# Performance work log

Hardware: AMD Instinct MI355X
Metric: run time of the kernel (lower is better)

The kernel has to match this reference:

```python
import jax, jax.numpy as jnp
import numpy as np

N, E, B, IN, H = 50000, 800000, 256, 1024, 256


def setup_inputs() -> dict:
    key = jax.random.key(0)
    ks = iter(jax.random.split(key, 40))
    w = lambda *s: jax.random.normal(next(ks), s, jnp.float32) * 0.05
    z = lambda *s: jnp.zeros(s, jnp.float32)
    inp = {
        "x": jax.random.normal(next(ks), (N, IN), jnp.float32),
        "edge_index": jax.random.randint(next(ks), (2, E), 0, N),
        "batch": jnp.sort(jax.random.randint(next(ks), (N,), 0, B)),
        "y": jax.random.randint(next(ks), (B,), 0, 2),
        "perm": jax.random.permutation(next(ks), B),
        # masker params
        "m_fc_w": w(IN, H), "m_fc_b": z(H),
        "m_c1_w": w(H, H), "m_c1_b": z(H),
        "m_c2_w": w(H, H), "m_c2_b": z(H),
        "m_node_w": w(H, 1), "m_node_b": z(1),
        "m_edge_w": w(2 * H, 1), "m_edge_b": z(1),
        # gnn_c params
        "c_fc_w": w(IN, H), "c_fc_b": z(H),
        "c_c1_w": w(H, H), "c_c1_b": z(H),
        "c_c2_w": w(H, H), "c_c2_b": z(H),
        # gnn_b params
        "b_fc_w": w(IN, H), "b_fc_b": z(H),
        "b_c1_w": w(H, H), "b_c1_b": z(H),
        "b_c2_w": w(H, H), "b_c2_b": z(H),
        # classifier heads
        "mlp_c_w": w(2 * H, 2), "mlp_c_b": z(2),
        "mlp_b_w": w(2 * H, 2), "mlp_b_b": z(2),
    }
    return inp


def _gcn_conv(x, w, b, row, col, ew):
    """PyG GCNConv: linear -> add self-loops -> sym-norm -> scatter-add -> bias."""
    n = x.shape[0]
    xw = x @ w
    loop = jnp.arange(n)
    r = jnp.concatenate([row, loop])
    c = jnp.concatenate([col, loop])
    if ew is None:
        ewf = jnp.ones(r.shape[0], xw.dtype)
    else:
        ewf = jnp.concatenate([ew, jnp.ones(n, xw.dtype)])
    deg = jax.ops.segment_sum(ewf, c, num_segments=n)
    dis = jnp.where(deg > 0, jax.lax.rsqrt(jnp.maximum(deg, 1e-12)), 0.0)
    norm = dis[r] * ewf * dis[c]
    out = jax.ops.segment_sum(xw[r] * norm[:, None], c, num_segments=n)
    return out + b


def _gnn_net(x, row, col, batch, node_mask, edge_mask, fc_w, fc_b, c1w, c1b, c2w, c2b):
    h = x * node_mask
    h = h @ fc_w + fc_b
    h = jax.nn.relu(_gcn_conv(h, c1w, c1b, row, col, edge_mask))
    h = jax.nn.relu(_gcn_conv(h, c2w, c2b, row, col, edge_mask))
    s = jax.ops.segment_sum(h, batch, num_segments=B)
    cnt = jax.ops.segment_sum(jnp.ones(h.shape[0], h.dtype), batch, num_segments=B)
    return s / jnp.maximum(cnt, 1.0)[:, None]


def _ce(logits, y):
    return -jnp.take_along_axis(jax.nn.log_softmax(logits, -1), y[:, None], 1)[:, 0]


def _gce(logits, y, q=0.7):
    p = jax.nn.softmax(logits, -1)
    yg = jnp.take_along_axis(p, y[:, None], 1)[:, 0]
    return _ce(logits, y) * (jax.lax.stop_gradient(yg) ** q) * q


def reference(x, edge_index, batch, y, perm,
              m_fc_w, m_fc_b, m_c1_w, m_c1_b, m_c2_w, m_c2_b,
              m_node_w, m_node_b, m_edge_w, m_edge_b,
              c_fc_w, c_fc_b, c_c1_w, c_c1_b, c_c2_w, c_c2_b,
              b_fc_w, b_fc_b, b_c1_w, b_c1_b, b_c2_w, b_c2_b,
              mlp_c_w, mlp_c_b, mlp_b_w, mlp_b_b):
    sg = jax.lax.stop_gradient
    row, col = edge_index[0], edge_index[1]

    # ---- GCNMasker (dropout = eval identity) ----
    h = x @ m_fc_w + m_fc_b
    h = jax.nn.relu(_gcn_conv(h, m_c1_w, m_c1_b, row, col, None))
    h = jax.nn.relu(_gcn_conv(h, m_c2_w, m_c2_b, row, col, None))
    node_score_c = jax.nn.sigmoid(h @ m_node_w + m_node_b)          # [N,1]
    # cat([x[row],x[col]]) @ W == (x @ W_top)[row] + (x @ W_bot)[col]
    es = (h @ m_edge_w[:H])[row] + (h @ m_edge_w[H:])[col] + m_edge_b
    edge_score_c = jax.nn.sigmoid(es)                               # [E,1]
    edge_score_b = 1.0 - edge_score_c
    node_score_b = 1.0 - node_score_c

    score_c = _gnn_net(x, row, col, batch, node_score_c, edge_score_c[:, 0],
                       c_fc_w, c_fc_b, c_c1_w, c_c1_b, c_c2_w, c_c2_b)  # [B,H]
    score_b = _gnn_net(x, row, col, batch, node_score_b, edge_score_b[:, 0],
                       b_fc_w, b_fc_b, b_c1_w, b_c1_b, b_c2_w, b_c2_b)  # [B,H]

    z_c = jnp.concatenate([score_c, sg(score_b)], axis=1)
    z_b = jnp.concatenate([sg(score_c), score_b], axis=1)
    pred_c = z_c @ mlp_c_w + mlp_c_b
    pred_b = z_b @ mlp_b_w + mlp_b_b

    loss_dis = _ce(pred_c, y).mean() + _gce(pred_b, y).mean()

    z_b_swap = score_b[perm]
    label_swap = y[perm]
    z_mix_conflict = jnp.concatenate([score_c, sg(z_b_swap)], axis=1)
    z_mix_align = jnp.concatenate([sg(score_c), z_b_swap], axis=1)
    pred_mix_conflict = z_mix_conflict @ mlp_c_w + mlp_c_b
    pred_mix_align = z_mix_align @ mlp_b_w + mlp_b_b
    loss_swap = _ce(pred_mix_conflict, y).mean() + _gce(pred_mix_align, label_swap).mean()

    lambda_swap = 15.0
    loss = loss_dis + lambda_swap * loss_swap
    return pred_c, loss
```

## Files before the change

### kernel.cpp

```cpp
#include <hip/hip_runtime.h>
#include <cstdint>
#include <cstddef>

#define N_NODES 50000
#define N_EDGES 800000
#define NB      256
#define IN_DIM  1024
#define HDIM    256

typedef __attribute__((ext_vector_type(8))) short bf16x8;
typedef __attribute__((ext_vector_type(4))) short s4v;
typedef __attribute__((ext_vector_type(4))) float f32x4;

__device__ __forceinline__ float sigmoidf_(float v) { return 1.0f / (1.0f + expf(-v)); }

__device__ __forceinline__ short f2bf(float f) {
    unsigned u = __float_as_uint(f);
    unsigned r = (u + 0x7FFFu + ((u >> 16) & 1u)) >> 16;
    return (short)r;
}
__device__ __forceinline__ float bf2f(short s) {
    return __uint_as_float(((unsigned)(unsigned short)s) << 16);
}

__global__ void k_hist(const int* __restrict__ col, int* __restrict__ cnt, int n) {
    int e = blockIdx.x * 256 + threadIdx.x;
    if (e < n) atomicAdd(&cnt[col[e]], 1);
}

__global__ void k_scan1(const int* __restrict__ cnt, int* __restrict__ ptr,
                        int* __restrict__ bsums, int n) {
    __shared__ int sh[256];
    int t = threadIdx.x;
    int base = blockIdx.x * 2048 + t * 8;
    int v[8]; int s = 0;
#pragma unroll
    for (int i = 0; i < 8; ++i) { int idx = base + i; v[i] = (idx < n) ? cnt[idx] : 0; s += v[i]; }
    sh[t] = s;
    __syncthreads();
    for (int off = 1; off < 256; off <<= 1) {
        int x = (t >= off) ? sh[t - off] : 0;
        __syncthreads();
        sh[t] += x;
        __syncthreads();
    }
    int excl = sh[t] - s;
    if (t == 255) bsums[blockIdx.x] = sh[255];
    int run = excl;
#pragma unroll
    for (int i = 0; i < 8; ++i) { int idx = base + i; if (idx < n) ptr[idx] = run; run += v[i]; }
}

__global__ void k_scan2(int* __restrict__ bsums, int nb, int* __restrict__ ptr_n) {
    if (threadIdx.x == 0 && blockIdx.x == 0) {
        int run = 0;
        for (int i = 0; i < nb; ++i) { int v = bsums[i]; bsums[i] = run; run += v; }
        ptr_n[0] = run;
    }
}

__global__ void k_scan3(int* __restrict__ ptr, const int* __restrict__ bsums, int n) {
    int base = blockIdx.x * 2048 + threadIdx.x * 8;
    int add = bsums[blockIdx.x];
#pragma unroll
    for (int i = 0; i < 8; ++i) { int idx = base + i; if (idx < n) ptr[idx] += add; }
}

__global__ void k_copy_int(const int* __restrict__ a, int* __restrict__ b, int n) {
    int i = blockIdx.x * 256 + threadIdx.x;
    if (i < n) b[i] = a[i];
}

__global__ void k_scatter(const int* __restrict__ row, const int* __restrict__ col,
                          int* __restrict__ fill, int* __restrict__ src,
                          int* __restrict__ eid, int n) {
    int e = blockIdx.x * 256 + threadIdx.x;
    if (e < n) {
        int c = col[e];
        int p = atomicAdd(&fill[c], 1);
        src[p] = row[e];
        eid[p] = e;
    }
}

__global__ void k_dis1(const int* __restrict__ ptr, float* __restrict__ dis, int n) {
    int i = blockIdx.x * 256 + threadIdx.x;
    if (i < n) {
        float deg = 1.0f + (float)(ptr[i + 1] - ptr[i]);
        dis[i] = 1.0f / sqrtf(deg);
    }
}

__global__ void k_splitB(const float* __restrict__ W, short* __restrict__ bt_hi,
                         short* __restrict__ bt_lo, int K) {
    int idx = blockIdx.x * 256 + threadIdx.x;
    if (idx >= 256 * (K >> 2)) return;
    int n = idx & 255, kq = (idx >> 8) << 2;
    s4v h, l;
#pragma unroll
    for (int j = 0; j < 4; ++j) {
        float v = W[(size_t)(kq + j) * 256 + n];
        short hh = f2bf(v);
        h[j] = hh;
        l[j] = f2bf(v - bf2f(hh));
    }
    *reinterpret_cast<s4v*>(&bt_hi[(size_t)n * K + kq]) = h;
    *reinterpret_cast<s4v*>(&bt_lo[(size_t)n * K + kq]) = l;
}

template <int AMODE, int OUT, int BIAS>
__global__ __launch_bounds__(256, 2) void k_gemm(const float* __restrict__ A32,
                                                 const short* __restrict__ AHg,
                                                 const short* __restrict__ ALg,
                                                 const short* __restrict__ BtHi,
                                                 const short* __restrict__ BtLo,
                                                 const float* __restrict__ bias,
                                                 float* __restrict__ C32,
                                                 short* __restrict__ CHg,
                                                 short* __restrict__ CLg,
                                                 int M, int K) {
    constexpr int LDT = 40;
    __shared__ short Ah[128 * LDT];
    __shared__ short Al[128 * LDT];
    __shared__ short Bh[128 * LDT];
    __shared__ short Bl[128 * LDT];

    int tid = threadIdx.x;
    int lane = tid & 63;
    int wave = tid >> 6;
    int wr = wave >> 1, wc = wave & 1;
    int lr = lane & 15, kg = lane >> 4;
    int m0 = blockIdx.y * 128, n0 = blockIdx.x * 128;

    f32x4 acc[4][4] = {};

    for (int k0 = 0; k0 < K; k0 += 32) {
        if constexpr (AMODE == 0) {
#pragma unroll
            for (int i = 0; i < 4; ++i) {
                int u = tid + i * 256;
                int rowi = u >> 3, kq = (u & 7) << 2;
                int gr = m0 + rowi;
                float4 av = make_float4(0.f, 0.f, 0.f, 0.f);
                if (gr < M) av = *reinterpret_cast<const float4*>(A32 + (size_t)gr * K + (k0 + kq));
                short hx = f2bf(av.x), hy = f2bf(av.y), hz = f2bf(av.z), hw = f2bf(av.w);
                s4v h = {hx, hy, hz, hw};
                s4v l = {f2bf(av.x - bf2f(hx)), f2bf(av.y - bf2f(hy)),
                         f2bf(av.z - bf2f(hz)), f2bf(av.w - bf2f(hw))};
                *reinterpret_cast<s4v*>(&Ah[rowi * LDT + kq]) = h;
                *reinterpret_cast<s4v*>(&Al[rowi * LDT + kq]) = l;
            }
        } else {
#pragma unroll
            for (int i = 0; i < 2; ++i) {
                int u = tid + i * 256;
                int rowi = u >> 2, kc = (u & 3) << 3;
                int gr = m0 + rowi;
                int4 h = make_int4(0, 0, 0, 0), l = make_int4(0, 0, 0, 0);
                if (gr < M) {
                    size_t g = (size_t)gr * K + k0 + kc;
                    h = *reinterpret_cast<const int4*>(AHg + g);
                    l = *reinterpret_cast<const int4*>(ALg + g);
                }
                *reinterpret_cast<int4*>(&Ah[rowi * LDT + kc]) = h;
                *reinterpret_cast<int4*>(&Al[rowi * LDT + kc]) = l;
            }
        }
#pragma unroll
        for (int i = 0; i < 2; ++i) {
            int u = tid + i * 256;
            int rowi = u >> 2, cq = (u & 3) << 3;
            const size_t g = (size_t)(n0 + rowi) * K + k0 + cq;
            int4 bh = *reinterpret_cast<const int4*>(BtHi + g);
            int4 bl = *reinterpret_cast<const int4*>(BtLo + g);
            *reinterpret_cast<int4*>(&Bh[rowi * LDT + cq]) = bh;
            *reinterpret_cast<int4*>(&Bl[rowi * LDT + cq]) = bl;
        }
        __syncthreads();

        bf16x8 a_h[4], a_l[4], b_h[4], b_l[4];
#pragma unroll
        for (int i = 0; i < 4; ++i) {
            int ar = wr * 64 + i * 16 + lr;
            a_h[i] = *reinterpret_cast<const bf16x8*>(&Ah[ar * LDT + kg * 8]);
            a_l[i] = *reinterpret_cast<const bf16x8*>(&Al[ar * LDT + kg * 8]);
            int br = wc * 64 + i * 16 + lr;
            b_h[i] = *reinterpret_cast<const bf16x8*>(&Bh[br * LDT + kg * 8]);
            b_l[i] = *reinterpret_cast<const bf16x8*>(&Bl[br * LDT + kg * 8]);
        }
#pragma unroll
        for (int i = 0; i < 4; ++i)
#pragma unroll
            for (int j = 0; j < 4; ++j) {
                acc[i][j] = __builtin_amdgcn_mfma_f32_16x16x32_bf16(a_h[i], b_h[j], acc[i][j], 0, 0, 0);
                acc[i][j] = __builtin_amdgcn_mfma_f32_16x16x32_bf16(a_h[i], b_l[j], acc[i][j], 0, 0, 0);
                acc[i][j] = __builtin_amdgcn_mfma_f32_16x16x32_bf16(a_l[i], b_h[j], acc[i][j], 0, 0, 0);
            }
        __syncthreads();
    }

#pragma unroll
    for (int i = 0; i < 4; ++i) {
#pragma unroll
        for (int j = 0; j < 4; ++j) {
#pragma unroll
            for (int r = 0; r < 4; ++r) {
                int gr = m0 + wr * 64 + i * 16 + kg * 4 + r;
                if (gr >= M) continue;
                int gc = n0 + wc * 64 + j * 16 + lr;
                float v = acc[i][j][r];
                if (BIAS) v += bias[gc];
                if constexpr (OUT == 0) {
                    C32[(size_t)gr * 256 + gc] = v;
                } else {
                    short h = f2bf(v);
                    CHg[(size_t)gr * 256 + gc] = h;
                    CLg[(size_t)gr * 256 + gc] = f2bf(v - bf2f(h));
                }
            }
        }
    }
}

template <int MODE, int OUT>
__global__ __launch_bounds__(256) void k_conv(const float* __restrict__ xw,
                                              const float* __restrict__ dis,
                                              const float* __restrict__ ew,
                                              const int* __restrict__ ptr,
                                              const int* __restrict__ srcA,
                                              const int* __restrict__ eidA,
                                              const float* __restrict__ bias,
                                              float* __restrict__ out32,
                                              short* __restrict__ outH,
                                              short* __restrict__ outL) {
    int node = blockIdx.x * 4 + (threadIdx.x >> 6);
    if (node >= N_NODES) return;
    int lane = threadIdx.x & 63;
    const float4* xw4 = reinterpret_cast<const float4*>(xw);
    int s = ptr[node], e = ptr[node + 1];
    float4 acc = make_float4(0.f, 0.f, 0.f, 0.f);
    int k = s;
    for (; k + 2 <= e; k += 2) {
        int sr0 = srcA[k], sr1 = srcA[k + 1];
        float w0 = dis[sr0], w1 = dis[sr1];
        if (MODE == 1) { w0 *= ew[eidA[k]]; w1 *= ew[eidA[k + 1]]; }
        else if (MODE == 2) { w0 *= (1.0f - ew[eidA[k]]); w1 *= (1.0f - ew[eidA[k + 1]]); }
        float4 v0 = xw4[(size_t)sr0 * 64 + lane];
        float4 v1 = xw4[(size_t)sr1 * 64 + lane];
        acc.x = fmaf(w1, v1.x, fmaf(w0, v0.x, acc.x));
        acc.y = fmaf(w1, v1.y, fmaf(w0, v0.y, acc.y));
        acc.z = fmaf(w1, v1.z, fmaf(w0, v0.z, acc.z));
        acc.w = fmaf(w1, v1.w, fmaf(w0, v0.w, acc.w));
    }
    if (k < e) {
        int sr = srcA[k];
        float w = dis[sr];
        if (MODE == 1) w *= ew[eidA[k]];
        else if (MODE == 2) w *= (1.0f - ew[eidA[k]]);
        float4 v = xw4[(size_t)sr * 64 + lane];
        acc.x = fmaf(w, v.x, acc.x);
        acc.y = fmaf(w, v.y, acc.y);
        acc.z = fmaf(w, v.z, acc.z);
        acc.w = fmaf(w, v.w, acc.w);
    }
    float di = dis[node];
    float4 xv = xw4[(size_t)node * 64 + lane];
    float4 bv = reinterpret_cast<const float4*>(bias)[lane];
    float ox = fmaxf(fmaf(di, acc.x + di * xv.x, bv.x), 0.0f);
    float oy = fmaxf(fmaf(di, acc.y + di * xv.y, bv.y), 0.0f);
    float oz = fmaxf(fmaf(di, acc.z + di * xv.z, bv.z), 0.0f);
    float ow = fmaxf(fmaf(di, acc.w + di * xv.w, bv.w), 0.0f);
    size_t o4 = (size_t)node * 64 + lane;
    if constexpr (OUT == 0) {
        reinterpret_cast<float4*>(out32)[o4] = make_float4(ox, oy, oz, ow);
    } else {
        short hx = f2bf(ox), hy = f2bf(oy), hz = f2bf(oz), hw = f2bf(ow);
        s4v h = {hx, hy, hz, hw};
        s4v l = {f2bf(ox - bf2f(hx)), f2bf(oy - bf2f(hy)),
                 f2bf(oz - bf2f(hz)), f2bf(ow - bf2f(hw))};
        reinterpret_cast<s4v*>(outH)[o4] = h;
        reinterpret_cast<s4v*>(outL)[o4] = l;
    }
}

__global__ __launch_bounds__(256) void k_nodescore(const float* __restrict__ h,
                                                   const float* __restrict__ node_w,
                                                   const float* __restrict__ node_b,
                                                   const float* __restrict__ edge_w,
                                                   float* __restrict__ ns,
                                                   float* __restrict__ en1,
                                                   float* __restrict__ en2) {
    int node = blockIdx.x * 4 + (threadIdx.x >> 6);
    if (node >= N_NODES) return;
    int lane = threadIdx.x & 63;
    float4 hv = reinterpret_cast<const float4*>(h)[(size_t)node * 64 + lane];
    float4 w1 = reinterpret_cast<const float4*>(node_w)[lane];
    float4 w2 = reinterpret_cast<const float4*>(edge_w)[lane];
    float4 w3 = reinterpret_cast<const float4*>(edge_w)[64 + lane];
    float d1 = hv.x * w1.x + hv.y * w1.y + hv.z * w1.z + hv.w * w1.w;
    float d2 = hv.x * w2.x + hv.y * w2.y + hv.z * w2.z + hv.w * w2.w;
    float d3 = hv.x * w3.x + hv.y * w3.y + hv.z * w3.z + hv.w * w3.w;
#pragma unroll
    for (int off = 32; off > 0; off >>= 1) {
        d1 += __shfl_xor(d1, off);
        d2 += __shfl_xor(d2, off);
        d3 += __shfl_xor(d3, off);
    }
    if (lane == 0) {
        ns[node] = sigmoidf_(d1 + node_b[0]);
        en1[node] = d2;
        en2[node] = d3;
    }
}

__global__ void k_edgescore(const int* __restrict__ row, const int* __restrict__ col,
                            const float* __restrict__ en1, const float* __restrict__ en2,
                            const float* __restrict__ eb, float* __restrict__ esc, int n) {
    int e = blockIdx.x * 256 + threadIdx.x;
    if (e < n) esc[e] = sigmoidf_(en1[row[e]] + en2[col[e]] + eb[0]);
}

__global__ void k_degcb(const int* __restrict__ ptr, const int* __restrict__ eidA,
                        const float* __restrict__ esc, float* __restrict__ dis_c,
                        float* __restrict__ dis_b, int n) {
    int i = blockIdx.x * 256 + threadIdx.x;
    if (i >= n) return;
    int s = ptr[i], e = ptr[i + 1];
    float t = 0.f;
    for (int k = s; k < e; ++k) t += esc[eidA[k]];
    float indeg = (float)(e - s);
    dis_c[i] = 1.0f / sqrtf(1.0f + t);
    dis_b[i] = 1.0f / sqrtf(1.0f + (indeg - t));
}

template <bool INV>
__global__ void k_scale(const float* __restrict__ A, const float* __restrict__ ns,
                        const float* __restrict__ bias,
                        short* __restrict__ oh, short* __restrict__ ol) {
    int idx = blockIdx.x * 256 + threadIdx.x;
    int node = idx >> 6, q = idx & 63;
    float s = ns[node];
    if (INV) s = 1.0f - s;
    float4 v = reinterpret_cast<const float4*>(A)[idx];
    float4 b = reinterpret_cast<const float4*>(bias)[q];
    float rx = fmaf(s, v.x, b.x), ry = fmaf(s, v.y, b.y);
    float rz = fmaf(s, v.z, b.z), rw = fmaf(s, v.w, b.w);
    short hx = f2bf(rx), hy = f2bf(ry), hz = f2bf(rz), hw = f2bf(rw);
    s4v h = {hx, hy, hz, hw};
    s4v l = {f2bf(rx - bf2f(hx)), f2bf(ry - bf2f(hy)),
             f2bf(rz - bf2f(hz)), f2bf(rw - bf2f(hw))};
    reinterpret_cast<s4v*>(oh)[idx] = h;
    reinterpret_cast<s4v*>(ol)[idx] = l;
}

__global__ void k_starts(const int* __restrict__ batch, int* __restrict__ starts) {
    int b = threadIdx.x;
    if (b > NB) return;
    int lo = 0, hi = N_NODES;
    while (lo < hi) { int mid = (lo + hi) >> 1; if (batch[mid] < b) lo = mid + 1; else hi = mid; }
    starts[b] = lo;
}

__global__ __launch_bounds__(256) void k_pool(const float* __restrict__ h,
                                              const int* __restrict__ starts,
                                              float* __restrict__ out) {
    int b = blockIdx.x, ch = threadIdx.x;
    int s = starts[b], e = starts[b + 1];
    float acc = 0.f;
    for (int i = s; i < e; ++i) acc += h[(size_t)i * HDIM + ch];
    out[b * HDIM + ch] = acc / fmaxf((float)(e - s), 1.0f);
}

__global__ __launch_bounds__(64) void k_head(const float* __restrict__ score_c,
                                             const float* __restrict__ score_b,
                                             const int* __restrict__ y,
                                             const int* __restrict__ perm,
                                             const float* __restrict__ wc,
                                             const float* __restrict__ bc,
                                             const float* __restrict__ wb,
                                             const float* __restrict__ bb,
                                             float* __restrict__ pred_out,
                                             float* __restrict__ loss_part) {
    int b = blockIdx.x, lane = threadIdx.x;
    int pidx = perm[b];
    float4 vc = reinterpret_cast<const float4*>(score_c)[b * 64 + lane];
    float4 vb = reinterpret_cast<const float4*>(score_b)[b * 64 + lane];
    float4 vp = reinterpret_cast<const float4*>(score_b)[pidx * 64 + lane];
    const float4* wc4 = reinterpret_cast<const float4*>(wc);
    const float4* wb4 = reinterpret_cast<const float4*>(wb);
    float4 cA0 = wc4[lane * 2], cA1 = wc4[lane * 2 + 1];
    float4 cB0 = wc4[128 + lane * 2], cB1 = wc4[128 + lane * 2 + 1];
    float4 bA0 = wb4[lane * 2], bA1 = wb4[lane * 2 + 1];
    float4 bB0 = wb4[128 + lane * 2], bB1 = wb4[128 + lane * 2 + 1];

    float c1_0 = vc.x * cA0.x + vc.y * cA0.z + vc.z * cA1.x + vc.w * cA1.z;
    float c1_1 = vc.x * cA0.y + vc.y * cA0.w + vc.z * cA1.y + vc.w * cA1.w;
    float c2_0 = vb.x * cB0.x + vb.y * cB0.z + vb.z * cB1.x + vb.w * cB1.z;
    float c2_1 = vb.x * cB0.y + vb.y * cB0.w + vb.z * cB1.y + vb.w * cB1.w;
    float cp_0 = vp.x * cB0.x + vp.y * cB0.z + vp.z * cB1.x + vp.w * cB1.z;
    float cp_1 = vp.x * cB0.y + vp.y * cB0.w + vp.z * cB1.y + vp.w * cB1.w;
    float b1_0 = vc.x * bA0.x + vc.y * bA0.z + vc.z * bA1.x + vc.w * bA1.z;
    float b1_1 = vc.x * bA0.y + vc.y * bA0.w + vc.z * bA1.y + vc.w * bA1.w;
    float b2_0 = vb.x * bB0.x + vb.y * bB0.z + vb.z * bB1.x + vb.w * bB1.z;
    float b2_1 = vb.x * bB0.y + vb.y * bB0.w + vb.z * bB1.y + vb.w * bB1.w;
    float bp_0 = vp.x * bB0.x + vp.y * bB0.z + vp.z * bB1.x + vp.w * bB1.z;
    float bp_1 = vp.x * bB0.y + vp.y * bB0.w + vp.z * bB1.y + vp.w * bB1.w;

#pragma unroll
    for (int off = 32; off > 0; off >>= 1) {
        c1_0 += __shfl_xor(c1_0, off); c1_1 += __shfl_xor(c1_1, off);
        c2_0 += __shfl_xor(c2_0, off); c2_1 += __shfl_xor(c2_1, off);
        cp_0 += __shfl_xor(cp_0, off); cp_1 += __shfl_xor(cp_1, off);
        b1_0 += __shfl_xor(b1_0, off); b1_1 += __shfl_xor(b1_1, off);
        b2_0 += __shfl_xor(b2_0, off); b2_1 += __shfl_xor(b2_1, off);
        bp_0 += __shfl_xor(bp_0, off); bp_1 += __shfl_xor(bp_1, off);
    }
    if (lane == 0) {
        float pc0 = c1_0 + c2_0 + bc[0], pc1 = c1_1 + c2_1 + bc[1];
        float pb0 = b1_0 + b2_0 + bb[0], pb1 = b1_1 + b2_1 + bb[1];
        float pmc0 = c1_0 + cp_0 + bc[0], pmc1 = c1_1 + cp_1 + bc[1];
        float pma0 = b1_0 + bp_0 + bb[0], pma1 = b1_1 + bp_1 + bb[1];
        int yy = y[b], yp = y[pidx];

        float m1 = fmaxf(pc0, pc1);
        float lse1 = m1 + logf(expf(pc0 - m1) + expf(pc1 - m1));
        float ce_c = lse1 - (yy == 0 ? pc0 : pc1);
        float m2 = fmaxf(pb0, pb1);
        float lse2 = m2 + logf(expf(pb0 - m2) + expf(pb1 - m2));
        float ly2 = (yy == 0 ? pb0 : pb1);
        float gce_b = (lse2 - ly2) * powf(expf(ly2 - lse2), 0.7f) * 0.7f;
        float m3 = fmaxf(pmc0, pmc1);
        float lse3 = m3 + logf(expf(pmc0 - m3) + expf(pmc1 - m3));
        float ce_mc = lse3 - (yy == 0 ? pmc0 : pmc1);
        float m4 = fmaxf(pma0, pma1);
        float lse4 = m4 + logf(expf(pma0 - m4) + expf(pma1 - m4));
        float ly4 = (yp == 0 ? pma0 : pma1);
        float gce_ma = (lse4 - ly4) * powf(expf(ly4 - lse4), 0.7f) * 0.7f;

        loss_part[b] = (ce_c + gce_b + 15.0f * (ce_mc + gce_ma)) * (1.0f / (float)NB);
        pred_out[b * 2 + 0] = pc0;
        pred_out[b * 2 + 1] = pc1;
    }
}

__global__ void k_lossred(const float* __restrict__ part, float* __restrict__ out) {
    __shared__ float sh[256];
    int t = threadIdx.x;
    sh[t] = part[t];
    __syncthreads();
    for (int off = 128; off > 0; off >>= 1) {
        if (t < off) sh[t] += sh[t + off];
        __syncthreads();
    }
    if (t == 0) out[0] = sh[0];
}

extern "C" void kernel_launch(void* const* d_in, const int* in_sizes, int n_in,
                              void* d_out, int out_size, void* d_ws, size_t ws_size,
                              hipStream_t stream) {
    (void)in_sizes; (void)n_in; (void)out_size; (void)ws_size;
    const float* x      = (const float*)d_in[0];
    const int*   ei     = (const int*)d_in[1];
    const int*   batch  = (const int*)d_in[2];
    const int*   y      = (const int*)d_in[3];
    const int*   perm   = (const int*)d_in[4];
    const float* m_fc_w = (const float*)d_in[5],  *m_fc_b = (const float*)d_in[6];
    const float* m_c1_w = (const float*)d_in[7],  *m_c1_b = (const float*)d_in[8];
    const float* m_c2_w = (const float*)d_in[9],  *m_c2_b = (const float*)d_in[10];
    const float* m_nd_w = (const float*)d_in[11], *m_nd_b = (const float*)d_in[12];
    const float* m_ed_w = (const float*)d_in[13], *m_ed_b = (const float*)d_in[14];
    const float* c_fc_w = (const float*)d_in[15], *c_fc_b = (const float*)d_in[16];
    const float* c_c1_w = (const float*)d_in[17], *c_c1_b = (const float*)d_in[18];
    const float* c_c2_w = (const float*)d_in[19], *c_c2_b = (const float*)d_in[20];
    const float* b_fc_w = (const float*)d_in[21], *b_fc_b = (const float*)d_in[22];
    const float* b_c1_w = (const float*)d_in[23], *b_c1_b = (const float*)d_in[24];
    const float* b_c2_w = (const float*)d_in[25], *b_c2_b = (const float*)d_in[26];
    const float* mlp_c_w = (const float*)d_in[27], *mlp_c_b = (const float*)d_in[28];
    const float* mlp_b_w = (const float*)d_in[29], *mlp_b_b = (const float*)d_in[30];
    const int* row = ei;
    const int* col = ei + N_EDGES;

    char* p = (char*)d_ws;
    auto alloc = [&](size_t bytes) -> void* {
        uintptr_t q = ((uintptr_t)p + 255) & ~(uintptr_t)255;
        p = (char*)(q + bytes);
        return (void*)q;
    };
    float* F1 = (float*)alloc((size_t)N_NODES * HDIM * 4);
    float* F2 = (float*)alloc((size_t)N_NODES * HDIM * 4);
    short* S1h = (short*)alloc((size_t)N_NODES * HDIM * 2);
    short* S1l = (short*)alloc((size_t)N_NODES * HDIM * 2);
    short* S2h = (short*)alloc((size_t)N_NODES * HDIM * 2);
    short* S2l = (short*)alloc((size_t)N_NODES * HDIM * 2);
    int* cnt    = (int*)alloc((size_t)N_NODES * 4);
    int* ptr    = (int*)alloc((size_t)(N_NODES + 1) * 4);
    int* bsums  = (int*)alloc(32 * 4);
    int* csrc   = (int*)alloc((size_t)N_EDGES * 4);
    int* ceid   = (int*)alloc((size_t)N_EDGES * 4);
    float* dis1 = (float*)alloc((size_t)N_NODES * 4);
    float* dis_c = (float*)alloc((size_t)N_NODES * 4);
    float* dis_b = (float*)alloc((size_t)N_NODES * 4);
    float* ns   = (float*)alloc((size_t)N_NODES * 4);
    float* en1  = (float*)alloc((size_t)N_NODES * 4);
    float* en2  = (float*)alloc((size_t)N_NODES * 4);
    float* esc  = (float*)alloc((size_t)N_EDGES * 4);
    float* sc   = (float*)alloc((size_t)NB * HDIM * 4);
    float* sb   = (float*)alloc((size_t)NB * HDIM * 4);
    int* starts = (int*)alloc((size_t)(NB + 1) * 4);
    float* lpart = (float*)alloc((size_t)NB * 4);
    short* wsp[9][2];
    const int wk[9] = {IN_DIM, HDIM, HDIM, IN_DIM, HDIM, HDIM, IN_DIM, HDIM, HDIM};
    for (int i = 0; i < 9; ++i) {
        wsp[i][0] = (short*)alloc((size_t)256 * wk[i] * 2);
        wsp[i][1] = (short*)alloc((size_t)256 * wk[i] * 2);
    }
    const float* wsrc[9] = {m_fc_w, m_c1_w, m_c2_w, c_fc_w, c_c1_w, c_c2_w,
                            b_fc_w, b_c1_w, b_c2_w};

    const int EB = N_EDGES / 256;
    const int NBk = (N_NODES + 255) / 256;
    const int NW = N_NODES / 4;
    const dim3 gG(2, (N_NODES + 127) / 128);

    hipMemsetAsync(cnt, 0, (size_t)N_NODES * 4, stream);
    k_hist<<<EB, 256, 0, stream>>>(col, cnt, N_EDGES);
    k_scan1<<<25, 256, 0, stream>>>(cnt, ptr, bsums, N_NODES);
    k_scan2<<<1, 64, 0, stream>>>(bsums, 25, ptr + N_NODES);
    k_scan3<<<25, 256, 0, stream>>>(ptr, bsums, N_NODES);
    k_copy_int<<<NBk, 256, 0, stream>>>(ptr, cnt, N_NODES);
    k_scatter<<<EB, 256, 0, stream>>>(row, col, cnt, csrc, ceid, N_EDGES);
    k_dis1<<<NBk, 256, 0, stream>>>(ptr, dis1, N_NODES);
    k_starts<<<1, 512, 0, stream>>>(batch, starts);
    for (int i = 0; i < 9; ++i)
        k_splitB<<<(256 * (wk[i] >> 2) + 255) / 256, 256, 0, stream>>>(
            wsrc[i], wsp[i][0], wsp[i][1], wk[i]);

    k_gemm<0, 1, 1><<<gG, 256, 0, stream>>>(x, nullptr, nullptr, wsp[0][0], wsp[0][1],
                                            m_fc_b, nullptr, S1h, S1l, N_NODES, IN_DIM);
    k_gemm<1, 0, 0><<<gG, 256, 0, stream>>>(nullptr, S1h, S1l, wsp[1][0], wsp[1][1],
                                            nullptr, F1, nullptr, nullptr, N_NODES, HDIM);
    k_conv<0, 1><<<NW, 256, 0, stream>>>(F1, dis1, nullptr, ptr, csrc, ceid, m_c1_b,
                                         nullptr, S2h, S2l);
    k_gemm<1, 0, 0><<<gG, 256, 0, stream>>>(nullptr, S2h, S2l, wsp[2][0], wsp[2][1],
                                            nullptr, F2, nullptr, nullptr, N_NODES, HDIM);
    k_conv<0, 0><<<NW, 256, 0, stream>>>(F2, dis1, nullptr, ptr, csrc, ceid, m_c2_b,
                                         F1, nullptr, nullptr);
    k_nodescore<<<NW, 256, 0, stream>>>(F1, m_nd_w, m_nd_b, m_ed_w, ns, en1, en2);
    k_edgescore<<<EB, 256, 0, stream>>>(row, col, en1, en2, m_ed_b, esc, N_EDGES);
    k_degcb<<<NBk, 256, 0, stream>>>(ptr, ceid, esc, dis_c, dis_b, N_NODES);

    k_gemm<0, 0, 0><<<gG, 256, 0, stream>>>(x, nullptr, nullptr, wsp[3][0], wsp[3][1],
                                            nullptr, F2, nullptr, nullptr, N_NODES, IN_DIM);
    k_scale<false><<<NW, 256, 0, stream>>>(F2, ns, c_fc_b, S1h, S1l);
    k_gemm<1, 0, 0><<<gG, 256, 0, stream>>>(nullptr, S1h, S1l, wsp[4][0], wsp[4][1],
                                            nullptr, F2, nullptr, nullptr, N_NODES, HDIM);
    k_conv<1, 1><<<NW, 256, 0, stream>>>(F2, dis_c, esc, ptr, csrc, ceid, c_c1_b,
                                         nullptr, S2h, S2l);
    k_gemm<1, 0, 0><<<gG, 256, 0, stream>>>(nullptr, S2h, S2l, wsp[5][0], wsp[5][1],
                                            nullptr, F2, nullptr, nullptr, N_NODES, HDIM);
    k_conv<1, 0><<<NW, 256, 0, stream>>>(F2, dis_c, esc, ptr, csrc, ceid, c_c2_b,
                                         F1, nullptr, nullptr);
    k_pool<<<NB, 256, 0, stream>>>(F1, starts, sc);

    k_gemm<0, 0, 0><<<gG, 256, 0, stream>>>(x, nullptr, nullptr, wsp[6][0], wsp[6][1],
                                            nullptr, F2, nullptr, nullptr, N_NODES, IN_DIM);
    k_scale<true><<<NW, 256, 0, stream>>>(F2, ns, b_fc_b, S1h, S1l);
    k_gemm<1, 0, 0><<<gG, 256, 0, stream>>>(nullptr, S1h, S1l, wsp[7][0], wsp[7][1],
                                            nullptr, F2, nullptr, nullptr, N_NODES, HDIM);
    k_conv<2, 1><<<NW, 256, 0, stream>>>(F2, dis_b, esc, ptr, csrc, ceid, b_c1_b,
                                         nullptr, S2h, S2l);
    k_gemm<1, 0, 0><<<gG, 256, 0, stream>>>(nullptr, S2h, S2l, wsp[8][0], wsp[8][1],
                                            nullptr, F2, nullptr, nullptr, N_NODES, HDIM);
    k_conv<2, 0><<<NW, 256, 0, stream>>>(F2, dis_b, esc, ptr, csrc, ceid, b_c2_b,
                                         F1, nullptr, nullptr);
    k_pool<<<NB, 256, 0, stream>>>(F1, starts, sb);

    float* outp = (float*)d_out;
    k_head<<<NB, 64, 0, stream>>>(sc, sb, y, perm, mlp_c_w, mlp_c_b, mlp_b_w, mlp_b_b,
                                  outp, lpart);
    k_lossred<<<1, 256, 0, stream>>>(lpart, outp + NB * 2);
}
```

Baseline: 2.302 ms.

## Batch three input-projection GEMMs into one pass and pipeline GEMM tile loads

The three x @ fc_w projections (masker, causal, bias branches) are merged into one GEMM over a concatenated 768-column weight, so the large x matrix is read and split into bf16 hi/lo once instead of three times. The node-mask scaling and fc bias are folded into the A-load of the following hidden GEMM, which removes the separate k_scale kernel. The GEMM main loop now prefetches the next K tile into registers while the MFMAs run, and shared memory switches from padded rows to an XOR-swizzled layout. The cost is more register pressure and an extra barrier per K step, which could reduce occupancy.

Result: no change. 2.304 ms (+0.1%).

```diff
diff --git a/kernel.cpp b/kernel.cpp
--- a/kernel.cpp
+++ b/kernel.cpp
@@ -92,7 +92,7 @@
 }
 
 __global__ void k_splitB(const float* __restrict__ W, short* __restrict__ bt_hi,
-                         short* __restrict__ bt_lo, int K) {
+                         short* __restrict__ bt_lo, int K, int nOff) {
     int idx = blockIdx.x * 256 + threadIdx.x;
     if (idx >= 256 * (K >> 2)) return;
     int n = idx & 255, kq = (idx >> 8) << 2;
@@ -104,37 +104,48 @@
         h[j] = hh;
         l[j] = f2bf(v - bf2f(hh));
     }
-    *reinterpret_cast<s4v*>(&bt_hi[(size_t)n * K + kq]) = h;
-    *reinterpret_cast<s4v*>(&bt_lo[(size_t)n * K + kq]) = l;
-}
-
-template <int AMODE, int OUT, int BIAS>
+    *reinterpret_cast<s4v*>(&bt_hi[(size_t)(nOff + n) * K + kq]) = h;
+    *reinterpret_cast<s4v*>(&bt_lo[(size_t)(nOff + n) * K + kq]) = l;
+}
+
+template <int AMODE, int SCALE, int OUTK>
 __global__ __launch_bounds__(256, 2) void k_gemm(const float* __restrict__ A32,
                                                  const short* __restrict__ AHg,
                                                  const short* __restrict__ ALg,
                                                  const short* __restrict__ BtHi,
                                                  const short* __restrict__ BtLo,
-                                                 const float* __restrict__ bias,
+                                                 const float* __restrict__ nsv,
+                                                 const float* __restrict__ kbias,
+                                                 const float* __restrict__ cbias,
                                                  float* __restrict__ C32,
                                                  short* __restrict__ CHg,
                                                  short* __restrict__ CLg,
+                                                 float* __restrict__ Cf1,
+                                                 float* __restrict__ Cf2,
                                                  int M, int K) {
-    constexpr int LDT = 40;
-    __shared__ short Ah[128 * LDT];
-    __shared__ short Al[128 * LDT];
-    __shared__ short Bh[128 * LDT];
-    __shared__ short Bl[128 * LDT];
-
-    int tid = threadIdx.x;
-    int lane = tid & 63;
-    int wave = tid >> 6;
-    int wr = wave >> 1, wc = wave & 1;
-    int lr = lane & 15, kg = lane >> 4;
-    int m0 = blockIdx.y * 128, n0 = blockIdx.x * 128;
+    __shared__ short Ah[128 * 32];
+    __shared__ short Al[128 * 32];
+    __shared__ short Bh[128 * 32];
+    __shared__ short Bl[128 * 32];
+
+    const int tid = threadIdx.x;
+    const int lane = tid & 63;
+    const int wave = tid >> 6;
+    const int wr = wave >> 1, wc = wave & 1;
+    const int lr = lane & 15, kg = lane >> 4;
+    const int m0 = blockIdx.y * 128, n0 = blockIdx.x * 128;
+    const int sw = (lr >> 1) & 3;
 
     f32x4 acc[4][4] = {};
 
-    for (int k0 = 0; k0 < K; k0 += 32) {
+    float4 pa[4]; float ps[4]; float4 pkb[4];
+    int4 pah[2], pal[2];
+    int4 pbh[2], pbl[2];
+
+    const int NT = K >> 5;
+
+    auto LOAD = [&](int t) {
+        const int k0 = t << 5;
         if constexpr (AMODE == 0) {
 #pragma unroll
             for (int i = 0; i < 4; ++i) {
@@ -142,51 +153,103 @@
                 int rowi = u >> 3, kq = (u & 7) << 2;
                 int gr = m0 + rowi;
                 float4 av = make_float4(0.f, 0.f, 0.f, 0.f);
-                if (gr < M) av = *reinterpret_cast<const float4*>(A32 + (size_t)gr * K + (k0 + kq));
+                float s = 1.f;
+                float4 kb = make_float4(0.f, 0.f, 0.f, 0.f);
+                if (gr < M) {
+                    av = *reinterpret_cast<const float4*>(A32 + (size_t)gr * K + k0 + kq);
+                    if constexpr (SCALE == 1) s = nsv[gr];
+                    if constexpr (SCALE == 2) s = 1.f - nsv[gr];
+                    if constexpr (SCALE != 0)
+                        kb = *reinterpret_cast<const float4*>(kbias + k0 + kq);
+                }
+                pa[i] = av; ps[i] = s; pkb[i] = kb;
+            }
+        } else {
+#pragma unroll
+            for (int i = 0; i < 2; ++i) {
+                int u = tid + i * 256;
+                int rowi = u >> 2, ch = u & 3;
+                int gr = m0 + rowi;
+                int4 h = make_int4(0, 0, 0, 0), l = make_int4(0, 0, 0, 0);
+                if (gr < M) {
+                    size_t g = (size_t)gr * K + k0 + (ch << 3);
+                    h = *reinterpret_cast<const int4*>(AHg + g);
+                    l = *reinterpret_cast<const int4*>(ALg + g);
+                }
+                pah[i] = h; pal[i] = l;
+            }
+        }
+#pragma unroll
+        for (int i = 0; i < 2; ++i) {
+            int u = tid + i * 256;
+            int rowi = u >> 2, ch = u & 3;
+            size_t g = (size_t)(n0 + rowi) * K + k0 + (ch << 3);
+            pbh[i] = *reinterpret_cast<const int4*>(BtHi + g);
+            pbl[i] = *reinterpret_cast<const int4*>(BtLo + g);
+        }
+    };
+
+    auto STORE = [&]() {
+        if constexpr (AMODE == 0) {
+#pragma unroll
+            for (int i = 0; i < 4; ++i) {
+                int u = tid + i * 256;
+                int rowi = u >> 3, kq = (u & 7) << 2;
+                float4 av = pa[i];
+                if constexpr (SCALE != 0) {
+                    float s = ps[i]; float4 kb = pkb[i];
+                    av.x = fmaf(s, av.x, kb.x);
+                    av.y = fmaf(s, av.y, kb.y);
+                    av.z = fmaf(s, av.z, kb.z);
+                    av.w = fmaf(s, av.w, kb.w);
+                }
                 short hx = f2bf(av.x), hy = f2bf(av.y), hz = f2bf(av.z), hw = f2bf(av.w);
                 s4v h = {hx, hy, hz, hw};
                 s4v l = {f2bf(av.x - bf2f(hx)), f2bf(av.y - bf2f(hy)),
                          f2bf(av.z - bf2f(hz)), f2bf(av.w - bf2f(hw))};
-                *reinterpret_cast<s4v*>(&Ah[rowi * LDT + kq]) = h;
-                *reinterpret_cast<s4v*>(&Al[rowi * LDT + kq]) = l;
+                int g = kq >> 3, hf = kq & 7;
+                int base = rowi * 32 + ((g ^ ((rowi >> 1) & 3)) << 3) + hf;
+                *reinterpret_cast<s4v*>(&Ah[base]) = h;
+                *reinterpret_cast<s4v*>(&Al[base]) = l;
             }
         } else {
 #pragma unroll
             for (int i = 0; i < 2; ++i) {
                 int u = tid + i * 256;
-                int rowi = u >> 2, kc = (u & 3) << 3;
-                int gr = m0 + rowi;
-                int4 h = make_int4(0, 0, 0, 0), l = make_int4(0, 0, 0, 0);
-                if (gr < M) {
-                    size_t g = (size_t)gr * K + k0 + kc;
-                    h = *reinterpret_cast<const int4*>(AHg + g);
-                    l = *reinterpret_cast<const int4*>(ALg + g);
-                }
-                *reinterpret_cast<int4*>(&Ah[rowi * LDT + kc]) = h;
-                *reinterpret_cast<int4*>(&Al[rowi * LDT + kc]) = l;
+                int rowi = u >> 2, ch = u & 3;
+                int base = rowi * 32 + ((ch ^ ((rowi >> 1) & 3)) << 3);
+                *reinterpret_cast<int4*>(&Ah[base]) = pah[i];
+                *reinterpret_cast<int4*>(&Al[base]) = pal[i];
             }
         }
 #pragma unroll
         for (int i = 0; i < 2; ++i) {
             int u = tid + i * 256;
-            int rowi = u >> 2, cq = (u & 3) << 3;
-            const size_t g = (size_t)(n0 + rowi) * K + k0 + cq;
-            int4 bh = *reinterpret_cast<const int4*>(BtHi + g);
-            int4 bl = *reinterpret_cast<const int4*>(BtLo + g);
-            *reinterpret_cast<int4*>(&Bh[rowi * LDT + cq]) = bh;
-            *reinterpret_cast<int4*>(&Bl[rowi * LDT + cq]) = bl;
+            int rowi = u >> 2, ch = u & 3;
+            int base = rowi * 32 + ((ch ^ ((rowi >> 1) & 3)) << 3);
+            *reinterpret_cast<int4*>(&Bh[base]) = pbh[i];
+            *reinterpret_cast<int4*>(&Bl[base]) = pbl[i];
         }
-        __syncthreads();
+    };
+
+    LOAD(0);
+    STORE();
+    __syncthreads();
+
+    for (int t = 0; t < NT; ++t) {
+        if (t + 1 < NT) LOAD(t + 1);
 
         bf16x8 a_h[4], a_l[4], b_h[4], b_l[4];
 #pragma unroll
         for (int i = 0; i < 4; ++i) {
             int ar = wr * 64 + i * 16 + lr;
-            a_h[i] = *reinterpret_cast<const bf16x8*>(&Ah[ar * LDT + kg * 8]);
-            a_l[i] = *reinterpret_cast<const bf16x8*>(&Al[ar * LDT + kg * 8]);
+            int aoff = ar * 32 + ((kg ^ sw) << 3);
+            a_h[i] = *reinterpret_cast<const bf16x8*>(&Ah[aoff]);
+            a_l[i] = *reinterpret_cast<const bf16x8*>(&Al[aoff]);
             int br = wc * 64 + i * 16 + lr;
-            b_h[i] = *reinterpret_cast<const bf16x8*>(&Bh[br * LDT + kg * 8]);
-            b_l[i] = *reinterpret_cast<const bf16x8*>(&Bl[br * LDT + kg * 8]);
+            int boff = br * 32 + ((kg ^ sw) << 3);
+            b_h[i] = *reinterpret_cast<const bf16x8*>(&Bh[boff]);
+            b_l[i] = *reinterpret_cast<const bf16x8*>(&Bl[boff]);
         }
 #pragma unroll
         for (int i = 0; i < 4; ++i)
@@ -197,6 +260,8 @@
                 acc[i][j] = __builtin_amdgcn_mfma_f32_16x16x32_bf16(a_l[i], b_h[j], acc[i][j], 0, 0, 0);
             }
         __syncthreads();
+        if (t + 1 < NT) STORE();
+        __syncthreads();
     }
 
 #pragma unroll
@@ -209,13 +274,20 @@
                 if (gr >= M) continue;
                 int gc = n0 + wc * 64 + j * 16 + lr;
                 float v = acc[i][j][r];
-                if (BIAS) v += bias[gc];
-                if constexpr (OUT == 0) {
+                if constexpr (OUTK == 0) {
                     C32[(size_t)gr * 256 + gc] = v;
                 } else {
-                    short h = f2bf(v);
-                    CHg[(size_t)gr * 256 + gc] = h;
-                    CLg[(size_t)gr * 256 + gc] = f2bf(v - bf2f(h));
+                    int seg = gc >> 8, c = gc & 255;
+                    if (seg == 0) {
+                        v += cbias[c];
+                        short h = f2bf(v);
+                        CHg[(size_t)gr * 256 + c] = h;
+                        CLg[(size_t)gr * 256 + c] = f2bf(v - bf2f(h));
+                    } else if (seg == 1) {
+                        Cf1[(size_t)gr * 256 + c] = v;
+                    } else {
+                        Cf2[(size_t)gr * 256 + c] = v;
+                    }
                 }
             }
         }
@@ -283,7 +355,8 @@
     }
 }
 
-__global__ __launch_bounds__(256) void k_nodescore(const float* __restrict__ h,
+__global__ __launch_bounds__(256) void k_nodescore(const short* __restrict__ Sh,
+                                                   const short* __restrict__ Sl,
                                                    const float* __restrict__ node_w,
                                                    const float* __restrict__ node_b,
                                                    const float* __restrict__ edge_w,
@@ -293,7 +366,11 @@
     int node = blockIdx.x * 4 + (threadIdx.x >> 6);
     if (node >= N_NODES) return;
     int lane = threadIdx.x & 63;
-    float4 hv = reinterpret_cast<const float4*>(h)[(size_t)node * 64 + lane];
+    size_t o4 = (size_t)node * 64 + lane;
+    s4v hh = reinterpret_cast<const s4v*>(Sh)[o4];
+    s4v hl = reinterpret_cast<const s4v*>(Sl)[o4];
+    float4 hv = make_float4(bf2f(hh[0]) + bf2f(hl[0]), bf2f(hh[1]) + bf2f(hl[1]),
+                            bf2f(hh[2]) + bf2f(hl[2]), bf2f(hh[3]) + bf2f(hl[3]));
     float4 w1 = reinterpret_cast<const float4*>(node_w)[lane];
     float4 w2 = reinterpret_cast<const float4*>(edge_w)[lane];
     float4 w3 = reinterpret_cast<const float4*>(edge_w)[64 + lane];
@@ -331,26 +408,6 @@
     float indeg = (float)(e - s);
     dis_c[i] = 1.0f / sqrtf(1.0f + t);
     dis_b[i] = 1.0f / sqrtf(1.0f + (indeg - t));
-}
-
-template <bool INV>
-__global__ void k_scale(const float* __restrict__ A, const float* __restrict__ ns,
-                        const float* __restrict__ bias,
-                        short* __restrict__ oh, short* __restrict__ ol) {
-    int idx = blockIdx.x * 256 + threadIdx.x;
-    int node = idx >> 6, q = idx & 63;
-    float s = ns[node];
-    if (INV) s = 1.0f - s;
-    float4 v = reinterpret_cast<const float4*>(A)[idx];
-    float4 b = reinterpret_cast<const float4*>(bias)[q];
-    float rx = fmaf(s, v.x, b.x), ry = fmaf(s, v.y, b.y);
-    float rz = fmaf(s, v.z, b.z), rw = fmaf(s, v.w, b.w);
-    short hx = f2bf(rx), hy = f2bf(ry), hz = f2bf(rz), hw = f2bf(rw);
-    s4v h = {hx, hy, hz, hw};
-    s4v l = {f2bf(rx - bf2f(hx)), f2bf(ry - bf2f(hy)),
-             f2bf(rz - bf2f(hz)), f2bf(rw - bf2f(hw))};
-    reinterpret_cast<s4v*>(oh)[idx] = h;
-    reinterpret_cast<s4v*>(ol)[idx] = l;
 }
 
 __global__ void k_starts(const int* __restrict__ batch, int* __restrict__ starts) {
@@ -486,12 +543,11 @@
         p = (char*)(q + bytes);
         return (void*)q;
     };
-    float* F1 = (float*)alloc((size_t)N_NODES * HDIM * 4);
-    float* F2 = (float*)alloc((size_t)N_NODES * HDIM * 4);
     short* S1h = (short*)alloc((size_t)N_NODES * HDIM * 2);
     short* S1l = (short*)alloc((size_t)N_NODES * HDIM * 2);
-    short* S2h = (short*)alloc((size_t)N_NODES * HDIM * 2);
-    short* S2l = (short*)alloc((size_t)N_NODES * HDIM * 2);
+    float* Fc  = (float*)alloc((size_t)N_NODES * HDIM * 4);
+    float* Fb  = (float*)alloc((size_t)N_NODES * HDIM * 4);
+    float* Dv  = (float*)alloc((size_t)N_NODES * HDIM * 4);
     int* cnt    = (int*)alloc((size_t)N_NODES * 4);
     int* ptr    = (int*)alloc((size_t)(N_NODES + 1) * 4);
     int* bsums  = (int*)alloc(32 * 4);
@@ -508,19 +564,20 @@
     float* sb   = (float*)alloc((size_t)NB * HDIM * 4);
     int* starts = (int*)alloc((size_t)(NB + 1) * 4);
     float* lpart = (float*)alloc((size_t)NB * 4);
-    short* wsp[9][2];
-    const int wk[9] = {IN_DIM, HDIM, HDIM, IN_DIM, HDIM, HDIM, IN_DIM, HDIM, HDIM};
-    for (int i = 0; i < 9; ++i) {
-        wsp[i][0] = (short*)alloc((size_t)256 * wk[i] * 2);
-        wsp[i][1] = (short*)alloc((size_t)256 * wk[i] * 2);
-    }
-    const float* wsrc[9] = {m_fc_w, m_c1_w, m_c2_w, c_fc_w, c_c1_w, c_c2_w,
-                            b_fc_w, b_c1_w, b_c2_w};
+    short* wfch = (short*)alloc((size_t)768 * IN_DIM * 2);
+    short* wfcl = (short*)alloc((size_t)768 * IN_DIM * 2);
+    short* hw[6][2];
+    for (int i = 0; i < 6; ++i) {
+        hw[i][0] = (short*)alloc((size_t)256 * HDIM * 2);
+        hw[i][1] = (short*)alloc((size_t)256 * HDIM * 2);
+    }
+    const float* hsrc[6] = {m_c1_w, m_c2_w, c_c1_w, c_c2_w, b_c1_w, b_c2_w};
 
     const int EB = N_EDGES / 256;
     const int NBk = (N_NODES + 255) / 256;
     const int NW = N_NODES / 4;
-    const dim3 gG(2, (N_NODES + 127) / 128);
+    const dim3 gFC(6, (N_NODES + 127) / 128);
+    const dim3 gH(2, (N_NODES + 127) / 128);
 
     hipMemsetAsync(cnt, 0, (size_t)N_NODES * 4, stream);
     k_hist<<<EB, 256, 0, stream>>>(col, cnt, N_EDGES);
@@ -531,49 +588,53 @@
     k_scatter<<<EB, 256, 0, stream>>>(row, col, cnt, csrc, ceid, N_EDGES);
     k_dis1<<<NBk, 256, 0, stream>>>(ptr, dis1, N_NODES);
     k_starts<<<1, 512, 0, stream>>>(batch, starts);
-    for (int i = 0; i < 9; ++i)
-        k_splitB<<<(256 * (wk[i] >> 2) + 255) / 256, 256, 0, stream>>>(
-            wsrc[i], wsp[i][0], wsp[i][1], wk[i]);
-
-    k_gemm<0, 1, 1><<<gG, 256, 0, stream>>>(x, nullptr, nullptr, wsp[0][0], wsp[0][1],
-                                            m_fc_b, nullptr, S1h, S1l, N_NODES, IN_DIM);
-    k_gemm<1, 0, 0><<<gG, 256, 0, stream>>>(nullptr, S1h, S1l, wsp[1][0], wsp[1][1],
-                                            nullptr, F1, nullptr, nullptr, N_NODES, HDIM);
-    k_conv<0, 1><<<NW, 256, 0, stream>>>(F1, dis1, nullptr, ptr, csrc, ceid, m_c1_b,
-                                         nullptr, S2h, S2l);
-    k_gemm<1, 0, 0><<<gG, 256, 0, stream>>>(nullptr, S2h, S2l, wsp[2][0], wsp[2][1],
-                                            nullptr, F2, nullptr, nullptr, N_NODES, HDIM);
-    k_conv<0, 0><<<NW, 256, 0, stream>>>(F2, dis1, nullptr, ptr, csrc, ceid, m_c2_b,
-                                         F1, nullptr, nullptr);
-    k_nodescore<<<NW, 256, 0, stream>>>(F1, m_nd_w, m_nd_b, m_ed_w, ns, en1, en2);
+    k_splitB<<<256, 256, 0, stream>>>(m_fc_w, wfch, wfcl, IN_DIM, 0);
+    k_splitB<<<256, 256, 0, stream>>>(c_fc_w, wfch, wfcl, IN_DIM, 256);
+    k_splitB<<<256, 256, 0, stream>>>(b_fc_w, wfch, wfcl, IN_DIM, 512);
+    for (int i = 0; i < 6; ++i)
+        k_splitB<<<64, 256, 0, stream>>>(hsrc[i], hw[i][0], hw[i][1], HDIM, 0);
+
+    k_gemm<0, 0, 2><<<gFC, 256, 0, stream>>>(x, nullptr, nullptr, wfch, wfcl,
+                                             nullptr, nullptr, m_fc_b,
+                                             nullptr, S1h, S1l, Fc, Fb, N_NODES, IN_DIM);
+
+    k_gemm<1, 0, 0><<<gH, 256, 0, stream>>>(nullptr, S1h, S1l, hw[0][0], hw[0][1],
+                                            nullptr, nullptr, nullptr,
+                                            Dv, nullptr, nullptr, nullptr, nullptr, N_NODES, HDIM);
+    k_conv<0, 1><<<NW, 256, 0, stream>>>(Dv, dis1, nullptr, ptr, csrc, ceid, m_c1_b,
+                                         nullptr, S1h, S1l);
+    k_gemm<1, 0, 0><<<gH, 256, 0, stream>>>(nullptr, S1h, S1l, hw[1][0], hw[1][1],
+                                            nullptr, nullptr, nullptr,
+                                            Dv, nullptr, nullptr, nullptr, nullptr, N_NODES, HDIM);
+    k_conv<0, 1><<<NW, 256, 0, stream>>>(Dv, dis1, nullptr, ptr, csrc, ceid, m_c2_b,
+                                         nullptr, S1h, S1l);
+    k_nodescore<<<NW, 256, 0, stream>>>(S1h, S1l, m_nd_w, m_nd_b, m_ed_w, ns, en1, en2);
     k_edgescore<<<EB, 256, 0, stream>>>(row, col, en1, en2, m_ed_b, esc, N_EDGES);
     k_degcb<<<NBk, 256, 0, stream>>>(ptr, ceid, esc, dis_c, dis_b, N_NODES);
 
-    k_gemm<0, 0, 0><<<gG, 256, 0, stream>>>(x, nullptr, nullptr, wsp[3][0], wsp[3][1],
-                                            nullptr, F2, nullptr, nullptr, N_NODES, IN_DIM);
-    k_scale<false><<<NW, 256, 0, stream>>>(F2, ns, c_fc_b, S1h, S1l);
-    k_gemm<1, 0, 0><<<gG, 256, 0, stream>>>(nullptr, S1h, S1l, wsp[4][0], wsp[4][1],
-                                            nullptr, F2, nullptr, nullptr, N_NODES, HDIM);
-    k_conv<1, 1><<<NW, 256, 0, stream>>>(F2, dis_c, esc, ptr, csrc, ceid, c_c1_b,
-                                         nullptr, S2h, S2l);
-    k_gemm<1, 0, 0><<<gG, 256, 0, stream>>>(nullptr, S2h, S2l, wsp[5][0], wsp[5][1],
-                                            nullptr, F2, nullptr, nullptr, N_NODES, HDIM);
-    k_conv<1, 0><<<NW, 256, 0, stream>>>(F2, dis_c, esc, ptr, csrc, ceid, c_c2_b,
-                                         F1, nullptr, nullptr);
-    k_pool<<<NB, 256, 0, stream>>>(F1, starts, sc);
-
-    k_gemm<0, 0, 0><<<gG, 256, 0, stream>>>(x, nullptr, nullptr, wsp[6][0], wsp[6][1],
-                                            nullptr, F2, nullptr, nullptr, N_NODES, IN_DIM);
-    k_scale<true><<<NW, 256, 0, stream>>>(F2, ns, b_fc_b, S1h, S1l);
-    k_gemm<1, 0, 0><<<gG, 256, 0, stream>>>(nullptr, S1h, S1l, wsp[7][0], wsp[7][1],
-                                            nullptr, F2, nullptr, nullptr, N_NODES, HDIM);
-    k_conv<2, 1><<<NW, 256, 0, stream>>>(F2, dis_b, esc, ptr, csrc, ceid, b_c1_b,
-                                         nullptr, S2h, S2l);
-    k_gemm<1, 0, 0><<<gG, 256, 0, stream>>>(nullptr, S2h, S2l, wsp[8][0], wsp[8][1],
-                                            nullptr, F2, nullptr, nullptr, N_NODES, HDIM);
-    k_conv<2, 0><<<NW, 256, 0, stream>>>(F2, dis_b, esc, ptr, csrc, ceid, b_c2_b,
-                                         F1, nullptr, nullptr);
-    k_pool<<<NB, 256, 0, stream>>>(F1, starts, sb);
+    k_gemm<0, 1, 0><<<gH, 256, 0, stream>>>(Fc, nullptr, nullptr, hw[2][0], hw[2][1],
+                                            ns, c_fc_b, nullptr,
+                                            Dv, nullptr, nullptr, nullptr, nullptr, N_NODES, HDIM);
+    k_conv<1, 1><<<NW, 256, 0, stream>>>(Dv, dis_c, esc, ptr, csrc, ceid, c_c1_b,
+                                         nullptr, S1h, S1l);
+    k_gemm<1, 0, 0><<<gH, 256, 0, stream>>>(nullptr, S1h, S1l, hw[3][0], hw[3][1],
+                                            nullptr, nullptr, nullptr,
+                                            Dv, nullptr, nullptr, nullptr, nullptr, N_NODES, HDIM);
+    k_conv<1, 0><<<NW, 256, 0, stream>>>(Dv, dis_c, esc, ptr, csrc, ceid, c_c2_b,
+                                         Fc, nullptr, nullptr);
+    k_pool<<<NB, 256, 0, stream>>>(Fc, starts, sc);
+
+    k_gemm<0, 2, 0><<<gH, 256, 0, stream>>>(Fb, nullptr, nullptr, hw[4][0], hw[4][1],
+                                            ns, b_fc_b, nullptr,
+                                            Dv, nullptr, nullptr, nullptr, nullptr, N_NODES, HDIM);
+    k_conv<2, 1><<<NW, 256, 0, stream>>>(Dv, dis_b, esc, ptr, csrc, ceid, b_c1_b,
+                                         nullptr, S1h, S1l);
+    k_gemm<1, 0, 0><<<gH, 256, 0, stream>>>(nullptr, S1h, S1l, hw[5][0], hw[5][1],
+                                            nullptr, nullptr, nullptr,
+                                            Dv, nullptr, nullptr, nullptr, nullptr, N_NODES, HDIM);
+    k_conv<2, 0><<<NW, 256, 0, stream>>>(Dv, dis_b, esc, ptr, csrc, ceid, b_c2_b,
+                                         Fb, nullptr, nullptr);
+    k_pool<<<NB, 256, 0, stream>>>(Fb, starts, sb);
 
     float* outp = (float*)d_out;
     k_head<<<NB, 64, 0, stream>>>(sc, sb, y, perm, mlp_c_w, mlp_c_b, mlp_b_w, mlp_b_b,
```
